# Performance work log

Hardware: AMD Instinct MI355X
Metric: run time of the kernel (lower is better)

## Reference

```python
import jax, jax.numpy as jnp
from jax import lax
import numpy as np

# Static module configuration (matches init_kwargs, idx=0)
B, T, H, W, C = 2, 8, 64, 64, 128
T_SP, H_SP, W_SP = 2, 64, 4          # idx=0 -> H_sp=resolution, W_sp=split_size
NUM_HEADS = 4
HEAD_DIM = C // NUM_HEADS
SCALE = HEAD_DIM ** -0.5
L = T * H * W
N = T_SP * H_SP * W_SP               # tokens per window = 512


def setup_inputs() -> dict:
    key = jax.random.key(0)
    k1, k2, k3 = jax.random.split(key, 3)
    return {
        "qkv": jax.random.normal(k1, (3, B, L, C), dtype=jnp.float32),
        "lepe_w": jax.random.normal(k2, (C, 1, 3, 3, 3), dtype=jnp.float32) * 0.05,  # depthwise Conv3d weight
        "lepe_b": jax.random.normal(k3, (C,), dtype=jnp.float32) * 0.05,
    }


def _to_windows(x):
    # x: (B, L, C) with L flattened as (T, H, W) -> (nW, N, C)
    x = x.reshape(B, T // T_SP, T_SP, H // H_SP, H_SP, W // W_SP, W_SP, C)
    x = x.transpose(0, 1, 3, 5, 2, 4, 6, 7)  # B, tB, hB, wB, T_sp, H_sp, W_sp, C
    return x.reshape(-1, N, C)


def reference(qkv, lepe_w, lepe_b):
    q, k, v = qkv[0], qkv[1], qkv[2]          # each (B, L, C)

    # q, k -> (nW, heads, N, head_dim)
    qw = _to_windows(q).reshape(-1, N, NUM_HEADS, HEAD_DIM).transpose(0, 2, 1, 3)
    kw = _to_windows(k).reshape(-1, N, NUM_HEADS, HEAD_DIM).transpose(0, 2, 1, 3)

    # v windows in NCDHW layout for the depthwise LePE conv: (nW, C, T_sp, H_sp, W_sp)
    v_sp = _to_windows(v).reshape(-1, T_SP, H_SP, W_SP, C).transpose(0, 4, 1, 2, 3)
    lepe = lax.conv_general_dilated(
        v_sp, lepe_w, window_strides=(1, 1, 1), padding='SAME',
        dimension_numbers=('NCDHW', 'OIDHW', 'NCDHW'), feature_group_count=C,
    ) + lepe_b[None, :, None, None, None]
    # match torch: reshape(-1, heads, head_dim, N).permute(0,1,3,2)
    lepe = lepe.reshape(-1, NUM_HEADS, HEAD_DIM, N).transpose(0, 1, 3, 2)
    vw = v_sp.reshape(-1, NUM_HEADS, HEAD_DIM, N).transpose(0, 1, 3, 2)

    # windowed attention (attn_drop = 0 in eval)
    attn = jax.nn.softmax(jnp.einsum('whnd,whmd->whnm', qw * SCALE, kw), axis=-1)
    out = jnp.einsum('whnm,whmd->whnd', attn, vw) + lepe     # (nW, heads, N, d)

    # merge heads and reverse window partition -> (B, L, C)
    out = out.transpose(0, 2, 1, 3).reshape(-1, N, C)
    out = out.reshape(B, T // T_SP, H // H_SP, W // W_SP, T_SP, H_SP, W_SP, C)
    out = out.transpose(0, 1, 4, 2, 5, 3, 6, 7).reshape(B, L, C)
    return out
```

## Files before the change

kernel.cpp:

```cpp
#include <hip/hip_runtime.h>
#include <hip/hip_fp16.h>

#define Bb 2
#define Tt 8
#define Hh 64
#define Ww 64
#define Cc 128
#define TSP 2
#define HSP 64
#define WSP 4
#define NH 4
#define HD 32
#define Ll (Tt*Hh*Ww)
#define Nn (TSP*HSP*WSP)
#define BLC (Bb*Ll*Cc)
#define QSCALE (0.17677669529663687f * 1.4426950408889634f)

typedef _Float16 half8_t __attribute__((ext_vector_type(8)));
typedef _Float16 half4_t __attribute__((ext_vector_type(4)));
typedef __fp16   fp16x4_t __attribute__((ext_vector_type(4)));
typedef __fp16   fp16x2_t __attribute__((ext_vector_type(2)));
typedef float   float4_t __attribute__((ext_vector_type(4)));

#if __has_builtin(__builtin_amdgcn_exp2f)
#define EXP2F(x) __builtin_amdgcn_exp2f(x)
#else
#define EXP2F(x) exp2f(x)
#endif

#define H4SPLAT(x) ((half4_t){(_Float16)(x), (_Float16)(x), (_Float16)(x), (_Float16)(x)})

__device__ __forceinline__ int l_of(int tB, int xB, int n) {
    return tB*8192 + xB*4 + (n & 3) + (n >> 2)*64;
}

__global__ __launch_bounds__(256, 2) void fused_attn_kernel(
    const float* __restrict__ qkv, const float* __restrict__ wgt,
    const float* __restrict__ bias, float* __restrict__ out)
{
    __shared__ _Float16 Vt[HD*Nn];

    const int bid = blockIdx.x;
    const int qh = bid & 1;
    const int wh_ = bid >> 1;
    const int w = wh_ >> 2, h = wh_ & 3;
    const int b = w >> 6, tB = (w >> 4) & 3, xB = w & 15;
    const int c0 = h*HD;
    const int t = threadIdx.x;
    const float* kg = qkv + BLC;
    const float* vg = qkv + 2*BLC;

    {
        const int d = t & 31, chb = t >> 5;
        for (int r = 0; r < 16; ++r) {
            int ch = r*8 + chb;
            int n0 = ch*4;
            int gi0 = (b*Ll + l_of(tB, xB, n0))*Cc + c0 + d;
            float f0 = vg[gi0];
            float f1 = vg[gi0 + Cc];
            float f2 = vg[gi0 + 2*Cc];
            float f3 = vg[gi0 + 3*Cc];
            half4_t hv;
            hv[0] = (_Float16)f0; hv[1] = (_Float16)f1;
            hv[2] = (_Float16)f2; hv[3] = (_Float16)f3;
            *(half4_t*)(Vt + d*512 + (ch ^ (d & 15))*4) = hv;
        }
    }

    const int wv = t >> 6, lane = t & 63;
    const int c = lane & 15, quad = lane >> 4;
    const int qbase = qh*256 + wv*64;
    half8_t qf[4];
    #pragma unroll
    for (int nt = 0; nt < 4; ++nt) {
        int q = qbase + nt*16 + c;
        int gi = (b*Ll + l_of(tB, xB, q))*Cc + c0 + quad*8;
        float4_t f0 = *(const float4_t*)(qkv + gi);
        float4_t f1 = *(const float4_t*)(qkv + gi + 4);
        half8_t qv;
        qv[0] = (_Float16)(f0.x*QSCALE); qv[1] = (_Float16)(f0.y*QSCALE);
        qv[2] = (_Float16)(f0.z*QSCALE); qv[3] = (_Float16)(f0.w*QSCALE);
        qv[4] = (_Float16)(f1.x*QSCALE); qv[5] = (_Float16)(f1.y*QSCALE);
        qv[6] = (_Float16)(f1.z*QSCALE); qv[7] = (_Float16)(f1.w*QSCALE);
        qf[nt] = qv;
    }
    __syncthreads();

    float4_t acc[2][4];
    float4_t lacc[4];
    const float4_t fzero = {0.f, 0.f, 0.f, 0.f};
    const float4_t cshift = {-4.f, -4.f, -4.f, -4.f};
    #pragma unroll
    for (int nt = 0; nt < 4; ++nt) {
        lacc[nt] = fzero;
        acc[0][nt] = fzero; acc[1][nt] = fzero;
    }

    const float* kp0 = kg + (b*Ll + l_of(tB, xB,      c))*Cc + c0 + quad*8;
    const float* kp1 = kg + (b*Ll + l_of(tB, xB, 16 + c))*Cc + c0 + quad*8;
    const int kstep = 512*Cc;

    float4_t kr0a = *(const float4_t*)(kp0);
    float4_t kr0b = *(const float4_t*)(kp0 + 4);
    float4_t kr1a = *(const float4_t*)(kp1);
    float4_t kr1b = *(const float4_t*)(kp1 + 4);

    for (int kb = 0; kb < 16; ++kb) {
        half8_t kf0, kf1;
        kf0[0] = (_Float16)kr0a.x; kf0[1] = (_Float16)kr0a.y;
        kf0[2] = (_Float16)kr0a.z; kf0[3] = (_Float16)kr0a.w;
        kf0[4] = (_Float16)kr0b.x; kf0[5] = (_Float16)kr0b.y;
        kf0[6] = (_Float16)kr0b.z; kf0[7] = (_Float16)kr0b.w;
        kf1[0] = (_Float16)kr1a.x; kf1[1] = (_Float16)kr1a.y;
        kf1[2] = (_Float16)kr1a.z; kf1[3] = (_Float16)kr1a.w;
        kf1[4] = (_Float16)kr1b.x; kf1[5] = (_Float16)kr1b.y;
        kf1[6] = (_Float16)kr1b.z; kf1[7] = (_Float16)kr1b.w;

        if (kb < 15) {
            kp0 += kstep; kp1 += kstep;
            kr0a = *(const float4_t*)(kp0);
            kr0b = *(const float4_t*)(kp0 + 4);
            kr1a = *(const float4_t*)(kp1);
            kr1b = *(const float4_t*)(kp1 + 4);
        }

        fp16x4_t vf[2][2];
        #pragma unroll
        for (int mi = 0; mi < 2; ++mi) {
            #pragma unroll
            for (int ks = 0; ks < 2; ++ks) {
                int dim = mi*16 + c;
                int ch = kb*8 + ks*4 + quad;
                vf[mi][ks] = *(const fp16x4_t*)(Vt + dim*512 + (ch ^ c)*4);
            }
        }

        #pragma unroll
        for (int nt = 0; nt < 4; ++nt) {
            float4_t s0 = __builtin_amdgcn_mfma_f32_16x16x32_f16(kf0, qf[nt], cshift, 0, 0, 0);
            float4_t s1 = __builtin_amdgcn_mfma_f32_16x16x32_f16(kf1, qf[nt], cshift, 0, 0, 0);
            float4_t e0, e1;
            e0.x = EXP2F(s0.x); e0.y = EXP2F(s0.y);
            e0.z = EXP2F(s0.z); e0.w = EXP2F(s0.w);
            e1.x = EXP2F(s1.x); e1.y = EXP2F(s1.y);
            e1.z = EXP2F(s1.z); e1.w = EXP2F(s1.w);
            lacc[nt] += e0;
            lacc[nt] += e1;
            fp16x2_t a0 = __builtin_amdgcn_cvt_pkrtz(e0.x, e0.y);
            fp16x2_t a1 = __builtin_amdgcn_cvt_pkrtz(e0.z, e0.w);
            fp16x2_t b0 = __builtin_amdgcn_cvt_pkrtz(e1.x, e1.y);
            fp16x2_t b1 = __builtin_amdgcn_cvt_pkrtz(e1.z, e1.w);
            fp16x4_t ph0, ph1;
            ph0[0] = a0[0]; ph0[1] = a0[1]; ph0[2] = a1[0]; ph0[3] = a1[1];
            ph1[0] = b0[0]; ph1[1] = b0[1]; ph1[2] = b1[0]; ph1[3] = b1[1];
            acc[0][nt] = __builtin_amdgcn_mfma_f32_16x16x16f16(vf[0][0], ph0, acc[0][nt], 0, 0, 0);
            acc[0][nt] = __builtin_amdgcn_mfma_f32_16x16x16f16(vf[0][1], ph1, acc[0][nt], 0, 0, 0);
            acc[1][nt] = __builtin_amdgcn_mfma_f32_16x16x16f16(vf[1][0], ph0, acc[1][nt], 0, 0, 0);
            acc[1][nt] = __builtin_amdgcn_mfma_f32_16x16x16f16(vf[1][1], ph1, acc[1][nt], 0, 0, 0);
        }
    }

    __syncthreads();
    {
        const int d  = t & 31;
        const int cb = t >> 5;
        _Float16 wh[27];
        #pragma unroll
        for (int tap = 0; tap < 27; ++tap)
            wh[tap] = (_Float16)wgt[(c0 + d)*27 + tap];
        _Float16 bh = (_Float16)bias[c0 + d];

        half4_t cacc[8];
        #pragma unroll
        for (int i = 0; i < 8; ++i) {
            int ch = qh*64 + cb*8 + i;
            int ts = ch >> 6, ys = ch & 63;
            half4_t acc4 = {bh, bh, bh, bh};
            #pragma unroll
            for (int dt = 0; dt < 3; ++dt) {
                int tt = ts + dt - 1;
                if ((unsigned)tt >= TSP) continue;
                #pragma unroll
                for (int dy = 0; dy < 3; ++dy) {
                    int yy = ys + dy - 1;
                    if ((unsigned)yy >= HSP) continue;
                    int sc = tt*64 + yy;
                    half4_t v4 = *(const half4_t*)(Vt + d*512 + (sc ^ (d & 15))*4);
                    half4_t sm = {(_Float16)0, v4[0], v4[1], v4[2]};
                    half4_t sp = {v4[1], v4[2], v4[3], (_Float16)0};
                    const int tb = dt*9 + dy*3;
                    acc4 += sm*H4SPLAT(wh[tb+0]) + v4*H4SPLAT(wh[tb+1]) + sp*H4SPLAT(wh[tb+2]);
                }
            }
            cacc[i] = acc4;
        }
        __syncthreads();
        #pragma unroll
        for (int i = 0; i < 8; ++i) {
            int ch = qh*64 + cb*8 + i;
            *(half4_t*)(Vt + d*512 + (ch ^ (d & 15))*4) = cacc[i];
        }
    }
    __syncthreads();

    #pragma unroll
    for (int nt = 0; nt < 4; ++nt) {
        float lpart = (lacc[nt].x + lacc[nt].y) + (lacc[nt].z + lacc[nt].w);
        lpart += __shfl_xor(lpart, 16, 64);
        lpart += __shfl_xor(lpart, 32, 64);
        float linv = 1.0f / lpart;
        int q = qbase + nt*16 + c;
        int chq = q >> 2, eq = q & 3;
        int gi = (b*Ll + l_of(tB, xB, q))*Cc + c0;
        #pragma unroll
        for (int mi = 0; mi < 2; ++mi) {
            float4_t r;
            #pragma unroll
            for (int rr = 0; rr < 4; ++rr) {
                int dl = quad*4 + rr;
                float lep = (float)Vt[(mi*16 + dl)*512 + (chq ^ dl)*4 + eq];
                r[rr] = acc[mi][nt][rr]*linv + lep;
            }
            *(float4_t*)(out + gi + mi*16 + quad*4) = r;
        }
    }
}

extern "C" void kernel_launch(void* const* d_in, const int* in_sizes, int n_in,
                              void* d_out, int out_size, void* d_ws, size_t ws_size,
                              hipStream_t stream) {
    const float* qkv  = (const float*)d_in[0];
    const float* wgt  = (const float*)d_in[1];
    const float* bias = (const float*)d_in[2];
    float* out = (float*)d_out;
    (void)d_ws; (void)ws_size; (void)in_sizes; (void)n_in; (void)out_size;

    hipLaunchKernelGGL(fused_attn_kernel, dim3(1024), dim3(256), 0, stream,
                       qkv, wgt, bias, out);
}
```

Measured before the change: 184.5 us.

## Compute softmax row sums with MFMA against ones and batch V loads

The softmax denominator is now accumulated by extra MFMA instructions that multiply the fp16 probability tiles by a ones matrix, replacing the per-element VALU adds and the final cross-lane shuffle reduction. The V staging loop is also restructured to issue eight strided global loads into registers before converting and storing them, to raise memory-level parallelism. The trade-off is two more MFMAs per tile, which add matrix-core work. The row sum is also taken from fp16-rounded probabilities rather than fp32 values, which slightly changes numerics.

```diff
diff --git a/kernel.cpp b/kernel.cpp
--- a/kernel.cpp
+++ b/kernel.cpp
@@ -52,18 +52,27 @@
 
     {
         const int d = t & 31, chb = t >> 5;
-        for (int r = 0; r < 16; ++r) {
-            int ch = r*8 + chb;
-            int n0 = ch*4;
-            int gi0 = (b*Ll + l_of(tB, xB, n0))*Cc + c0 + d;
-            float f0 = vg[gi0];
-            float f1 = vg[gi0 + Cc];
-            float f2 = vg[gi0 + 2*Cc];
-            float f3 = vg[gi0 + 3*Cc];
-            half4_t hv;
-            hv[0] = (_Float16)f0; hv[1] = (_Float16)f1;
-            hv[2] = (_Float16)f2; hv[3] = (_Float16)f3;
-            *(half4_t*)(Vt + d*512 + (ch ^ (d & 15))*4) = hv;
+        #pragma unroll
+        for (int half = 0; half < 2; ++half) {
+            float4_t fb[8];
+            #pragma unroll
+            for (int r = 0; r < 8; ++r) {
+                int ch = (half*8 + r)*8 + chb;
+                int n0 = ch*4;
+                const float* p = vg + (b*Ll + l_of(tB, xB, n0))*Cc + c0 + d;
+                fb[r][0] = p[0];
+                fb[r][1] = p[Cc];
+                fb[r][2] = p[2*Cc];
+                fb[r][3] = p[3*Cc];
+            }
+            #pragma unroll
+            for (int r = 0; r < 8; ++r) {
+                int ch = (half*8 + r)*8 + chb;
+                half4_t hv;
+                hv[0] = (_Float16)fb[r][0]; hv[1] = (_Float16)fb[r][1];
+                hv[2] = (_Float16)fb[r][2]; hv[3] = (_Float16)fb[r][3];
+                *(half4_t*)(Vt + d*512 + (ch ^ (d & 15))*4) = hv;
+            }
         }
     }
 
@@ -87,12 +96,13 @@
     __syncthreads();
 
     float4_t acc[2][4];
-    float4_t lacc[4];
+    float4_t acc_l[4];
     const float4_t fzero = {0.f, 0.f, 0.f, 0.f};
     const float4_t cshift = {-4.f, -4.f, -4.f, -4.f};
+    const fp16x4_t ones16 = {(__fp16)1.f, (__fp16)1.f, (__fp16)1.f, (__fp16)1.f};
     #pragma unroll
     for (int nt = 0; nt < 4; ++nt) {
-        lacc[nt] = fzero;
+        acc_l[nt] = fzero;
         acc[0][nt] = fzero; acc[1][nt] = fzero;
     }
 
@@ -144,8 +154,6 @@
             e0.z = EXP2F(s0.z); e0.w = EXP2F(s0.w);
             e1.x = EXP2F(s1.x); e1.y = EXP2F(s1.y);
             e1.z = EXP2F(s1.z); e1.w = EXP2F(s1.w);
-            lacc[nt] += e0;
-            lacc[nt] += e1;
             fp16x2_t a0 = __builtin_amdgcn_cvt_pkrtz(e0.x, e0.y);
             fp16x2_t a1 = __builtin_amdgcn_cvt_pkrtz(e0.z, e0.w);
             fp16x2_t b0 = __builtin_amdgcn_cvt_pkrtz(e1.x, e1.y);
@@ -157,6 +165,8 @@
             acc[0][nt] = __builtin_amdgcn_mfma_f32_16x16x16f16(vf[0][1], ph1, acc[0][nt], 0, 0, 0);
             acc[1][nt] = __builtin_amdgcn_mfma_f32_16x16x16f16(vf[1][0], ph0, acc[1][nt], 0, 0, 0);
             acc[1][nt] = __builtin_amdgcn_mfma_f32_16x16x16f16(vf[1][1], ph1, acc[1][nt], 0, 0, 0);
+            acc_l[nt] = __builtin_amdgcn_mfma_f32_16x16x16f16(ones16, ph0, acc_l[nt], 0, 0, 0);
+            acc_l[nt] = __builtin_amdgcn_mfma_f32_16x16x16f16(ones16, ph1, acc_l[nt], 0, 0, 0);
         }
     }
 
@@ -205,10 +215,7 @@
 
     #pragma unroll
     for (int nt = 0; nt < 4; ++nt) {
-        float lpart = (lacc[nt].x + lacc[nt].y) + (lacc[nt].z + lacc[nt].w);
-        lpart += __shfl_xor(lpart, 16, 64);
-        lpart += __shfl_xor(lpart, 32, 64);
-        float linv = 1.0f / lpart;
+        float linv = 1.0f / acc_l[nt].x;
         int q = qbase + nt*16 + c;
         int chq = q >> 2, eq = q & 3;
         int gi = (b*Ll + l_of(tB, xB, q))*Cc + c0;
```

New measurement: 181.2 us. No clear change (-1.8%).
